# Performance work log

Measured on AMD Instinct MI355X. Metric: run time of the kernel, lower is better.

The kernel has to match this reference:

```python
import jax, jax.numpy as jnp
import numpy as np

# Static problem sizes (uniform graphs for jit-friendliness)
B = 64          # number of hypergraphs in the batch
N_PER = 32      # shape-nodes per hypergraph (num_nodes_hgraph, uniform)
D_ID = 256      # shape_id_dim
D_MULT = 64     # shape_multiplicity_dim
LATENT = 512    # latent_dim
D_NODE = D_ID + D_MULT           # 320
FEAT = 3 * D_NODE + LATENT       # 1472, MLP input dim
HID = 2 * FEAT                   # 2944
NUM_ATOMS = 11                   # 1 + feature_sizes['num_atoms']
VOCAB_ID, VOCAB_MULT = 100, 20


def setup_inputs() -> dict:
    key = jax.random.key(0)
    ks = jax.random.split(key, 11)
    s1 = 1.0 / np.sqrt(FEAT)
    s2 = 1.0 / np.sqrt(HID)
    s3 = 1.0 / np.sqrt(FEAT)
    return {
        "shape_node_idx": jax.random.randint(ks[0], (B * N_PER,), 0, VOCAB_ID),
        "shape_node_mult": jax.random.randint(ks[1], (B * N_PER,), 0, VOCAB_MULT),
        "z_graph": jax.random.normal(ks[2], (B, LATENT), jnp.float32),
        "id_emb": jax.random.normal(ks[3], (VOCAB_ID, D_ID), jnp.float32) * 0.02,
        "mult_emb": jax.random.normal(ks[4], (VOCAB_MULT, D_MULT), jnp.float32) * 0.02,
        "W1": jax.random.normal(ks[5], (FEAT, HID), jnp.float32) * s1,
        "b1": jnp.zeros((HID,), jnp.float32),
        "W2": jax.random.normal(ks[6], (HID, FEAT), jnp.float32) * s2,
        "b2": jnp.zeros((FEAT,), jnp.float32),
        "W3": jax.random.normal(ks[7], (FEAT, NUM_ATOMS), jnp.float32) * s3,
        "b3": jnp.zeros((NUM_ATOMS,), jnp.float32),
    }


def reference(shape_node_idx, shape_node_mult, z_graph, id_emb, mult_emb,
              W1, b1, W2, b2, W3, b3):
    # Node features: concat of shape-id and multiplicity embeddings -> [B, n, d_node]
    x = jnp.concatenate([id_emb[shape_node_idx], mult_emb[shape_node_mult]], axis=-1)
    x = x.reshape(B, N_PER, D_NODE)

    # Per-graph segment aggregation (node_aggregation='mean') -> [B, d_node]
    agg = x.mean(axis=1)

    # All intra-graph node pairs (block-diagonal edge pattern), edge (i, j):
    # input = [x_i, x_j, z_graph, agg] broadcast to [B, n, n, FEAT]
    xi = jnp.broadcast_to(x[:, :, None, :], (B, N_PER, N_PER, D_NODE))
    xj = jnp.broadcast_to(x[:, None, :, :], (B, N_PER, N_PER, D_NODE))
    zg = jnp.broadcast_to(z_graph[:, None, None, :], (B, N_PER, N_PER, LATENT))
    ag = jnp.broadcast_to(agg[:, None, None, :], (B, N_PER, N_PER, D_NODE))
    feat = jnp.concatenate([xi, xj, zg, ag], axis=-1)  # [B, n, n, FEAT]

    # MLP [FEAT, 2*FEAT, FEAT, NUM_ATOMS] with ReLU activations
    h = jax.nn.relu(jnp.einsum('bijf,fh->bijh', feat, W1) + b1)
    h = jax.nn.relu(jnp.einsum('bijh,hf->bijf', h, W2) + b2)
    logits = jnp.einsum('bijf,fa->bija', h, W3) + b3  # [B, n, n, A]

    # _to_symmetric: average each edge value with its transpose
    logits = 0.5 * (logits + jnp.swapaxes(logits, 1, 2))

    # Flattened per-edge logits (matches sparse COO value order: row-major pairs)
    return logits.reshape(B * N_PER * N_PER, NUM_ATOMS)
```

## Files before the change

### kernel.cpp

```cpp
#include <hip/hip_runtime.h>
#include <stdint.h>

#define NBG   64
#define NPER  32
#define DNODE 320
#define FEAT  1472
#define HIDN  2944
#define FEATP 1536
#define NA    11
#define NROWS 2048
#define MEDGE 65536

typedef __attribute__((ext_vector_type(8))) short    bf16x8;
typedef __attribute__((ext_vector_type(4))) float    fv4;
typedef __attribute__((ext_vector_type(2))) float    fv2;
typedef __attribute__((ext_vector_type(4))) unsigned uiv4;

__device__ __forceinline__ unsigned short f2bf(float f) {
  unsigned u = __builtin_bit_cast(unsigned, f);
  u += 0x7fffu + ((u >> 16) & 1u);
  return (unsigned short)(u >> 16);
}
__device__ __forceinline__ float bf2f(unsigned short h) {
  unsigned u = ((unsigned)h) << 16;
  return __builtin_bit_cast(float, u);
}
__device__ __forceinline__ unsigned cvt_pk_bf16(float lo, float hi) {
  unsigned r;
  asm("v_cvt_pk_bf16_f32 %0, %1, %2" : "=v"(r) : "v"(lo), "v"(hi));
  return r;
}
__device__ __forceinline__ fv2 pk_add(fv2 a, fv2 b) {
  fv2 d;
  asm("v_pk_add_f32 %0, %1, %2" : "=v"(d) : "v"(a), "v"(b));
  return d;
}
__device__ __forceinline__ unsigned pk_relu2(unsigned x, unsigned z) {
  unsigned r;
  asm("v_pk_max_i16 %0, %1, %2" : "=v"(r) : "v"(x), "v"(z));
  return r;
}
__device__ __forceinline__ fv2 lo2(fv4 v) { return __builtin_shufflevector(v, v, 0, 1); }
__device__ __forceinline__ fv2 hi2(fv4 v) { return __builtin_shufflevector(v, v, 2, 3); }
__device__ __forceinline__ void gload_lds16(const void* g, void* l) {
  __builtin_amdgcn_global_load_lds((const __attribute__((address_space(1))) void*)g,
                                   (__attribute__((address_space(3))) void*)l, 16, 0, 0);
}

__global__ void k_transpose_bf16(const float* __restrict__ src, unsigned short* __restrict__ dst,
                                 int K, int N, int Npad) {
  __shared__ float tile[64][65];
  int k0 = blockIdx.x * 64, n0 = blockIdx.y * 64;
  int r = threadIdx.x >> 2, cb = (threadIdx.x & 3) * 16;
  const float* srow = src + (size_t)(k0 + r) * N + n0 + cb;
#pragma unroll
  for (int c = 0; c < 16; ++c) {
    int n = n0 + cb + c;
    tile[r][cb + c] = (n < N) ? srow[c] : 0.f;
  }
  __syncthreads();
  unsigned short* drow = dst + (size_t)(n0 + r) * K + k0 + cb;
#pragma unroll
  for (int c = 0; c < 16; ++c) drow[c] = f2bf(tile[cb + c][r]);
}

__global__ void k_embed(const int* __restrict__ idx, const int* __restrict__ mlt,
                        const float* __restrict__ id_emb, const float* __restrict__ mult_emb,
                        unsigned short* __restrict__ xb) {
  int t = blockIdx.x, c = threadIdx.x;
  int iv = idx[t], mv = mlt[t];
  xb[t * DNODE + c] = f2bf(id_emb[iv * 256 + c]);
  if (c < 64) xb[t * DNODE + 256 + c] = f2bf(mult_emb[mv * 64 + c]);
}

__global__ void k_agg(const unsigned short* __restrict__ xb, float* __restrict__ agg) {
  int b = blockIdx.x;
  for (int d = threadIdx.x; d < DNODE; d += 256) {
    float s = 0.f;
    for (int i = 0; i < NPER; ++i) s += bf2f(xb[(b * NPER + i) * DNODE + d]);
    agg[b * DNODE + d] = s * (1.f / 32.f);
  }
}

__global__ void k_za(const float* __restrict__ z, const float* __restrict__ agg,
                     unsigned short* __restrict__ za) {
  int b = blockIdx.x;
  for (int c = threadIdx.x; c < 832; c += 256) {
    unsigned short v = 0;
    if (b < NBG) v = (c < 512) ? f2bf(z[b * 512 + c]) : f2bf(agg[b * DNODE + (c - 512)]);
    za[b * 832 + c] = v;
  }
}

__global__ void k_gemm1(const unsigned short* __restrict__ A, int sA, int Mrows,
                        const unsigned short* __restrict__ W1T, int kOff, int Ksteps,
                        float* __restrict__ C, const float* __restrict__ bias) {
  __shared__ alignas(16) unsigned short Als[128 * 32];
  __shared__ alignas(16) unsigned short Bls[128 * 32];
  int bx = blockIdx.x;
  int mt = bx / 23, nc = bx - mt * 23;
  int m0 = mt * 128, n0 = nc * 128;
  int tid = threadIdx.x, lane = tid & 63, w = tid >> 6;

  fv4 acc[4][4] = {};
  for (int kt = 0; kt < Ksteps; ++kt) {
    int k0 = kt * 32;
    __syncthreads();
#pragma unroll
    for (int q = 0; q < 2; ++q) {
      int seg = w * 2 + q;
      int row = seg * 16 + (lane >> 2);
      int col = (lane & 3) * 8;
      gload_lds16(A + (size_t)(m0 + row) * sA + k0 + col, &Als[seg * 512]);
      gload_lds16(W1T + (size_t)(n0 + row) * FEAT + kOff + k0 + col, &Bls[seg * 512]);
    }
    __syncthreads();
    bf16x8 aF[4], bF[4];
#pragma unroll
    for (int mf = 0; mf < 4; ++mf)
      aF[mf] = *(const bf16x8*)&Als[((w >> 1) * 64 + mf * 16 + (lane & 15)) * 32 + (lane >> 4) * 8];
#pragma unroll
    for (int nf = 0; nf < 4; ++nf)
      bF[nf] = *(const bf16x8*)&Bls[((w & 1) * 64 + nf * 16 + (lane & 15)) * 32 + (lane >> 4) * 8];
#pragma unroll
    for (int mf = 0; mf < 4; ++mf)
#pragma unroll
      for (int nf = 0; nf < 4; ++nf)
        acc[mf][nf] = __builtin_amdgcn_mfma_f32_16x16x32_bf16(aF[mf], bF[nf], acc[mf][nf], 0, 0, 0);
  }
  int mq = (w >> 1) * 64, nq = (w & 1) * 64;
#pragma unroll
  for (int mf = 0; mf < 4; ++mf)
#pragma unroll
    for (int nf = 0; nf < 4; ++nf) {
      int n = n0 + nq + nf * 16 + (lane & 15);
      float bv = bias ? bias[n] : 0.f;
#pragma unroll
      for (int r = 0; r < 4; ++r) {
        int m = m0 + mq + mf * 16 + (lane >> 4) * 4 + r;
        if (m < Mrows) C[(size_t)m * HIDN + n] = acc[mf][nf][r] + bv;
      }
    }
}

__global__ void k_pq(float* __restrict__ P1, const float* __restrict__ Q) {
  int r = blockIdx.x;
  const float* q = Q + (size_t)(r >> 5) * HIDN;
  float* p = P1 + (size_t)r * HIDN;
  for (int n = threadIdx.x; n < HIDN; n += 256) p[n] += q[n];
}

__global__ void k_zero(float* __restrict__ p, int n) {
  int i = blockIdx.x * 256 + threadIdx.x;
  if (i < n) p[i] = 0.f;
}

__global__ __launch_bounds__(256, 2)
void k_gemm2(const float* __restrict__ PQ1, const float* __restrict__ P2,
             const unsigned short* __restrict__ W2T,
             const float* __restrict__ b2, const float* __restrict__ W3,
             float* __restrict__ Lout) {
  __shared__ alignas(16) unsigned char LB[43008];
  int raw = blockIdx.x;
  int g = (raw & 7) * 384 + (raw >> 3);
  int nc2 = g / 512;
  int mt  = g - nc2 * 512;
  int m0 = mt * 128, n0 = nc2 * 256;
  int tid = threadIdx.x, lane = tid & 63, w = tid >> 6;
  int bG = m0 >> 10;
  int i0 = (m0 >> 5) & 31;
  int ks = lane >> 4;
  int r  = lane & 15;

  const int swcolB = ((lane & 3) ^ ((lane >> 3) & 3)) * 8;
  const int swcolP = (((lane >> 1) & 3) ^ ((lane >> 3) & 3)) * 8 + (lane & 1) * 4;

  auto STAGEB = [&](int kt, int buf) {
#pragma unroll
    for (int q = 0; q < 4; ++q) {
      int seg = w * 4 + q;
      int row = seg * 16 + (lane >> 2);
      gload_lds16(W2T + (size_t)(n0 + row) * HIDN + kt * 32 + swcolB,
                  LB + buf * 16384 + seg * 1024);
    }
  };
  auto STAGESRC = [&](int kt, int buf) {
    gload_lds16(P2 + (size_t)(bG * NPER + 8 * w + (lane >> 3)) * HIDN + kt * 32 + swcolP,
                LB + 32768 + buf * 4096 + w * 1024);
    if (w == 0)
      gload_lds16(PQ1 + (size_t)(bG * NPER + i0 + (lane >> 3)) * HIDN + kt * 32 + (lane & 7) * 4,
                  LB + 40960 + buf * 1024);
  };

  fv4 acc[4][8] = {};
  unsigned z0 = 0;
  asm volatile("" : "+v"(z0));

  STAGEB(0, 0);
  STAGESRC(0, 0);
  __syncthreads();

  int il0 = (w >> 1) * 2;
  for (int kt = 0; kt < 92; ++kt) {
    int cur = kt & 1, nxt = cur ^ 1;
    if (kt < 91) { STAGEB(kt + 1, nxt); STAGESRC(kt + 1, nxt); }

    const unsigned char* Bb = LB + cur * 16384;
    const unsigned char* Pb = LB + 32768 + cur * 4096;
    const unsigned char* Qb = LB + 40960 + cur * 1024;

    int psw = (ks ^ (r & 3)) * 32;
    fv4 q0[2], q1[2], p0[2], p1[2];
#pragma unroll
    for (int h = 0; h < 2; ++h) {
      q0[h] = *(const fv4*)(Qb + il0 * 128 + ks * 32 + h * 16);
      q1[h] = *(const fv4*)(Qb + (il0 + 1) * 128 + ks * 32 + h * 16);
      p0[h] = *(const fv4*)(Pb + r * 128 + psw + h * 16);
      p1[h] = *(const fv4*)(Pb + (16 + r) * 128 + psw + h * 16);
    }
    bf16x8 bF[8];
#pragma unroll
    for (int nf = 0; nf < 8; ++nf) {
      int brow = (w & 1) * 128 + nf * 16 + r;
      int slot = ks ^ ((brow >> 1) & 3);
      bF[nf] = *(const bf16x8*)(Bb + brow * 64 + slot * 16);
    }

    bf16x8 aF[4];
#pragma unroll
    for (int mf = 0; mf < 4; ++mf) {
      fv4 qa0 = (mf & 2) ? q1[0] : q0[0];
      fv4 qa1 = (mf & 2) ? q1[1] : q0[1];
      fv4 pa0 = (mf & 1) ? p1[0] : p0[0];
      fv4 pa1 = (mf & 1) ? p1[1] : p0[1];
      fv2 s00 = pk_add(lo2(qa0), lo2(pa0));
      fv2 s01 = pk_add(hi2(qa0), hi2(pa0));
      fv2 s10 = pk_add(lo2(qa1), lo2(pa1));
      fv2 s11 = pk_add(hi2(qa1), hi2(pa1));
      uiv4 u;
      u[0] = pk_relu2(cvt_pk_bf16(s00[0], s00[1]), z0);
      u[1] = pk_relu2(cvt_pk_bf16(s01[0], s01[1]), z0);
      u[2] = pk_relu2(cvt_pk_bf16(s10[0], s10[1]), z0);
      u[3] = pk_relu2(cvt_pk_bf16(s11[0], s11[1]), z0);
      aF[mf] = __builtin_bit_cast(bf16x8, u);
    }

#pragma unroll
    for (int nf = 0; nf < 8; ++nf)
#pragma unroll
      for (int mf = 0; mf < 4; ++mf)
        acc[mf][nf] = __builtin_amdgcn_mfma_f32_16x16x32_bf16(aF[mf], bF[nf], acc[mf][nf], 0, 0, 0);
    __syncthreads();
  }

  float* red = (float*)LB;
  int nq = (w & 1) * 128;
#pragma unroll
  for (int mf = 0; mf < 4; ++mf) {
    float s[4][NA];
#pragma unroll
    for (int rr = 0; rr < 4; ++rr)
#pragma unroll
      for (int a = 0; a < NA; ++a) s[rr][a] = 0.f;
#pragma unroll
    for (int nf = 0; nf < 8; ++nf) {
      int n = n0 + nq + nf * 16 + r;
      if (n < FEAT) {
        float bv = b2[n];
        float w3r[NA];
#pragma unroll
        for (int a = 0; a < NA; ++a) w3r[a] = W3[n * NA + a];
#pragma unroll
        for (int rr = 0; rr < 4; ++rr) {
          float h = fmaxf(acc[mf][nf][rr] + bv, 0.f);
#pragma unroll
          for (int a = 0; a < NA; ++a) s[rr][a] += h * w3r[a];
        }
      }
    }
#pragma unroll
    for (int off = 1; off < 16; off <<= 1)
#pragma unroll
      for (int rr = 0; rr < 4; ++rr)
#pragma unroll
        for (int a = 0; a < NA; ++a) s[rr][a] += __shfl_xor(s[rr][a], off, 64);
    int a = r;
    if (a < NA) {
#pragma unroll
      for (int rr = 0; rr < 4; ++rr)
        red[w * 704 + (mf * 16 + ks * 4 + rr) * NA + a] = s[rr][a];
    }
  }
  __syncthreads();
  for (int e = tid; e < 128 * NA; e += 256) {
    int row = e / NA, a = e - row * NA;
    int wr = row >> 6, rr = row & 63;
    float v = red[(wr * 2 + 0) * 704 + rr * NA + a] + red[(wr * 2 + 1) * 704 + rr * NA + a];
    atomicAdd(&Lout[(size_t)(m0 + row) * NA + a], v);
  }
}

__global__ void k_sym(const float* __restrict__ Lraw, const float* __restrict__ b3,
                      float* __restrict__ out) {
  int e = blockIdx.x * 256 + threadIdx.x;
  if (e >= MEDGE * NA) return;
  int m = e / NA, a = e - m * NA;
  int msw = (m & ~1023) | ((m & 31) << 5) | ((m >> 5) & 31);
  out[e] = 0.5f * (Lraw[e] + Lraw[(size_t)msw * NA + a]) + b3[a];
}

extern "C" void kernel_launch(void* const* d_in, const int* in_sizes, int n_in,
                              void* d_out, int out_size, void* d_ws, size_t ws_size,
                              hipStream_t stream) {
  const int*   idx      = (const int*)d_in[0];
  const int*   mlt      = (const int*)d_in[1];
  const float* z        = (const float*)d_in[2];
  const float* id_emb   = (const float*)d_in[3];
  const float* mult_emb = (const float*)d_in[4];
  const float* W1       = (const float*)d_in[5];
  const float* b1       = (const float*)d_in[6];
  const float* W2       = (const float*)d_in[7];
  const float* b2       = (const float*)d_in[8];
  const float* W3       = (const float*)d_in[9];
  const float* b3       = (const float*)d_in[10];
  float* out = (float*)d_out;

  uint8_t* ws = (uint8_t*)d_ws;
  size_t o = 0;
  auto alloc = [&](size_t bytes) { size_t r = o; o += (bytes + 255) & ~(size_t)255; return r; };
  size_t oW1T = alloc((size_t)HIDN * FEAT * 2);
  size_t oW2T = alloc((size_t)FEATP * HIDN * 2);
  size_t oXB  = alloc((size_t)NROWS * DNODE * 2);
  size_t oZA  = alloc((size_t)128 * 832 * 2);
  size_t oAG  = alloc((size_t)NBG * DNODE * 4);
  size_t oP1  = alloc((size_t)NROWS * HIDN * 4);
  size_t oP2  = alloc((size_t)NROWS * HIDN * 4);
  size_t oQ   = alloc((size_t)NBG * HIDN * 4);
  size_t oLR  = alloc((size_t)MEDGE * NA * 4);
  if (ws_size < o) return;

  unsigned short* W1T = (unsigned short*)(ws + oW1T);
  unsigned short* W2T = (unsigned short*)(ws + oW2T);
  unsigned short* xb  = (unsigned short*)(ws + oXB);
  unsigned short* za  = (unsigned short*)(ws + oZA);
  float* agg = (float*)(ws + oAG);
  float* P1  = (float*)(ws + oP1);
  float* P2  = (float*)(ws + oP2);
  float* Qm  = (float*)(ws + oQ);
  float* LR  = (float*)(ws + oLR);

  k_transpose_bf16<<<dim3(FEAT / 64, HIDN / 64), 256, 0, stream>>>(W1, W1T, FEAT, HIDN, HIDN);
  k_transpose_bf16<<<dim3(HIDN / 64, FEATP / 64), 256, 0, stream>>>(W2, W2T, HIDN, FEAT, FEATP);
  k_embed<<<NROWS, 256, 0, stream>>>(idx, mlt, id_emb, mult_emb, xb);
  k_agg<<<NBG, 256, 0, stream>>>(xb, agg);
  k_za<<<128, 256, 0, stream>>>(z, agg, za);
  k_gemm1<<<16 * 23, 256, 0, stream>>>(xb, DNODE, NROWS, W1T, 0, 10, P1, nullptr);
  k_gemm1<<<16 * 23, 256, 0, stream>>>(xb, DNODE, NROWS, W1T, 320, 10, P2, nullptr);
  k_gemm1<<<1 * 23, 256, 0, stream>>>(za, 832, NBG, W1T, 640, 26, Qm, b1);
  k_pq<<<NROWS, 256, 0, stream>>>(P1, Qm);
  k_zero<<<(MEDGE * NA + 255) / 256, 256, 0, stream>>>(LR, MEDGE * NA);
  k_gemm2<<<512 * 6, 256, 0, stream>>>(P1, P2, W2T, b2, W3, LR);
  k_sym<<<(MEDGE * NA + 255) / 256, 256, 0, stream>>>(LR, b3, out);
}
```

Baseline: 1.133 ms.

## Triple-buffer LDS stages and software-pipeline A-fragment construction in gemm2

```diff
diff --git a/kernel.cpp b/kernel.cpp
--- a/kernel.cpp
+++ b/kernel.cpp
@@ -160,7 +160,7 @@
              const unsigned short* __restrict__ W2T,
              const float* __restrict__ b2, const float* __restrict__ W3,
              float* __restrict__ Lout) {
-  __shared__ alignas(16) unsigned char LB[43008];
+  __shared__ alignas(16) unsigned char LB[64512];
   int raw = blockIdx.x;
   int g = (raw & 7) * 384 + (raw >> 3);
   int nc2 = g / 512;
@@ -171,6 +171,7 @@
   int i0 = (m0 >> 5) & 31;
   int ks = lane >> 4;
   int r  = lane & 15;
+  int il0 = (w >> 1) * 2;
 
   const int swcolB = ((lane & 3) ^ ((lane >> 3) & 3)) * 8;
   const int swcolP = (((lane >> 1) & 3) ^ ((lane >> 3) & 3)) * 8 + (lane & 1) * 4;
@@ -186,29 +187,19 @@
   };
   auto STAGESRC = [&](int kt, int buf) {
     gload_lds16(P2 + (size_t)(bG * NPER + 8 * w + (lane >> 3)) * HIDN + kt * 32 + swcolP,
-                LB + 32768 + buf * 4096 + w * 1024);
+                LB + 49152 + buf * 4096 + w * 1024);
     if (w == 0)
       gload_lds16(PQ1 + (size_t)(bG * NPER + i0 + (lane >> 3)) * HIDN + kt * 32 + (lane & 7) * 4,
-                  LB + 40960 + buf * 1024);
+                  LB + 61440 + buf * 1024);
   };
 
   fv4 acc[4][8] = {};
   unsigned z0 = 0;
   asm volatile("" : "+v"(z0));
 
-  STAGEB(0, 0);
-  STAGESRC(0, 0);
-  __syncthreads();
-
-  int il0 = (w >> 1) * 2;
-  for (int kt = 0; kt < 92; ++kt) {
-    int cur = kt & 1, nxt = cur ^ 1;
-    if (kt < 91) { STAGEB(kt + 1, nxt); STAGESRC(kt + 1, nxt); }
-
-    const unsigned char* Bb = LB + cur * 16384;
-    const unsigned char* Pb = LB + 32768 + cur * 4096;
-    const unsigned char* Qb = LB + 40960 + cur * 1024;
-
+  auto CONSTRUCT = [&](int buf, bf16x8 (&aF)[4]) {
+    const unsigned char* Pb = LB + 49152 + buf * 4096;
+    const unsigned char* Qb = LB + 61440 + buf * 1024;
     int psw = (ks ^ (r & 3)) * 32;
     fv4 q0[2], q1[2], p0[2], p1[2];
 #pragma unroll
@@ -218,15 +209,6 @@
       p0[h] = *(const fv4*)(Pb + r * 128 + psw + h * 16);
       p1[h] = *(const fv4*)(Pb + (16 + r) * 128 + psw + h * 16);
     }
-    bf16x8 bF[8];
-#pragma unroll
-    for (int nf = 0; nf < 8; ++nf) {
-      int brow = (w & 1) * 128 + nf * 16 + r;
-      int slot = ks ^ ((brow >> 1) & 3);
-      bF[nf] = *(const bf16x8*)(Bb + brow * 64 + slot * 16);
-    }
-
-    bf16x8 aF[4];
 #pragma unroll
     for (int mf = 0; mf < 4; ++mf) {
       fv4 qa0 = (mf & 2) ? q1[0] : q0[0];
@@ -244,13 +226,41 @@
       u[3] = pk_relu2(cvt_pk_bf16(s11[0], s11[1]), z0);
       aF[mf] = __builtin_bit_cast(bf16x8, u);
     }
-
+  };
+
+  auto STEP = [&](int kt, bf16x8 (&cur)[4], bf16x8 (&nxt)[4]) {
+    if (kt < 90) {
+      int sb = (kt + 2) % 3;
+      STAGEB(kt + 2, sb);
+      STAGESRC(kt + 2, sb);
+    }
+    const unsigned char* Bb = LB + (kt % 3) * 16384;
+    bf16x8 bF[8];
+#pragma unroll
+    for (int nf = 0; nf < 8; ++nf) {
+      int brow = (w & 1) * 128 + nf * 16 + r;
+      int slot = ks ^ ((brow >> 1) & 3);
+      bF[nf] = *(const bf16x8*)(Bb + brow * 64 + slot * 16);
+    }
 #pragma unroll
     for (int nf = 0; nf < 8; ++nf)
 #pragma unroll
       for (int mf = 0; mf < 4; ++mf)
-        acc[mf][nf] = __builtin_amdgcn_mfma_f32_16x16x32_bf16(aF[mf], bF[nf], acc[mf][nf], 0, 0, 0);
+        acc[mf][nf] = __builtin_amdgcn_mfma_f32_16x16x32_bf16(cur[mf], bF[nf], acc[mf][nf], 0, 0, 0);
+    if (kt < 91) CONSTRUCT((kt + 1) % 3, nxt);
     __syncthreads();
+  };
+
+  STAGEB(0, 0); STAGESRC(0, 0);
+  STAGEB(1, 1); STAGESRC(1, 1);
+  __syncthreads();
+
+  bf16x8 aA[4], aB[4];
+  CONSTRUCT(0, aA);
+
+  for (int kt = 0; kt < 92; kt += 2) {
+    STEP(kt, aA, aB);
+    STEP(kt + 1, aB, aA);
   }
 
   float* red = (float*)LB;
```

Measured after the change: 1.161 ms. +2.5%, slower.
